# Kernel optimization log

Hardware: AMD Instinct MI355X
Metric: run time of the kernel (lower is better)

The kernel has to match this reference:

```python
import jax, jax.numpy as jnp
import numpy as np

HEADS = 8
DIM_HEAD = 64
SCALE = DIM_HEAD ** -0.5


def setup_inputs() -> dict:
    key = jax.random.key(0)
    k1, k2, k3, k4 = jax.random.split(key, 4)
    b, dim, l = 4, 512, 2048
    hidden = HEADS * DIM_HEAD  # 512
    x = jax.random.normal(k1, (b, dim, l), dtype=jnp.float32)
    w_qkv = jax.random.normal(k2, (3 * hidden, dim), dtype=jnp.float32) * (dim ** -0.5)
    w_out = jax.random.normal(k3, (dim, hidden), dtype=jnp.float32) * (hidden ** -0.5)
    b_out = jax.random.normal(k4, (dim,), dtype=jnp.float32) * 0.01
    return {"x": x, "w_qkv": w_qkv, "w_out": w_out, "b_out": b_out}


def reference(x, w_qkv, w_out, b_out):
    b, c, l = x.shape
    h, d = HEADS, DIM_HEAD
    # 1x1 Conv1d == channel matmul: [3*hidden, c] x [b, c, l] -> [b, 3*hidden, l]
    qkv = jnp.einsum('oc,bcl->bol', w_qkv, x)
    q, k, v = jnp.split(qkv, 3, axis=1)
    # 'b (h d) l -> b h d l'
    q = q.reshape(b, h, d, l) * SCALE
    k = k.reshape(b, h, d, l)
    v = v.reshape(b, h, d, l)
    sim = jnp.einsum('bhdi,bhdj->bhij', q, k)          # [b, h, l, l]
    attn = jax.nn.softmax(sim, axis=-1)
    out = jnp.einsum('bhij,bhdj->bhid', attn, v)       # [b, h, l, d]
    # 'b h l d -> b (h d) l'
    out = out.transpose(0, 1, 3, 2).reshape(b, h * d, l)
    return jnp.einsum('oc,bcl->bol', w_out, out) + b_out[None, :, None]
```

## Files before the change

kernel.cpp:

```cpp
#include <hip/hip_runtime.h>

#define L_SEQ 2048
#define KDIM  512

typedef __attribute__((ext_vector_type(8))) short short8v;
typedef __attribute__((ext_vector_type(4))) float f32x4;

static __device__ __forceinline__ short f2b(float f) {
    union { float f; unsigned u; } v; v.f = f;
    unsigned r = v.u + 0x7fffu + ((v.u >> 16) & 1u);
    return (short)(r >> 16);
}

static __device__ __forceinline__ float fast_exp2(float x) {
#if __has_builtin(__builtin_amdgcn_exp2f)
    return __builtin_amdgcn_exp2f(x);
#else
    return exp2f(x);
#endif
}

static __device__ __forceinline__ void gl2lds16(const short* g, short* l) {
    __builtin_amdgcn_global_load_lds(
        (const __attribute__((address_space(1))) unsigned*)g,
        (__attribute__((address_space(3))) unsigned*)l,
        16, 0, 0);
}

__global__ __launch_bounds__(256) void prep(
    const float* __restrict__ wq, const float* __restrict__ wo,
    const float* __restrict__ x,
    short* __restrict__ wqb, short* __restrict__ wob, short* __restrict__ xT)
{
    __shared__ __align__(16) float T[64 * 72];
    const int t = threadIdx.x;
    int bid = blockIdx.x;

    if (bid < 1024) {
        const int i = bid * 256 + t;
        const int NQ = 1536 * 512 / 4;
        float4 v;
        if (i < NQ) v = ((const float4*)wq)[i];
        else        v = ((const float4*)wo)[i - NQ];
        short4 s;
        s.x = f2b(v.x); s.y = f2b(v.y); s.z = f2b(v.z); s.w = f2b(v.w);
        if (i < NQ) ((short4*)wqb)[i] = s;
        else        ((short4*)wob)[i - NQ] = s;
        return;
    }
    bid -= 1024;
    const int l0 = (bid & 31) * 64;
    const int c0 = ((bid >> 5) & 7) * 64;
    const int b  = bid >> 8;

#pragma unroll
    for (int j = 0; j < 4; ++j) {
        const int idx = j * 256 + t;
        const int row = idx >> 4, c4 = idx & 15;
        const float4 v = *(const float4*)&x[((size_t)b * KDIM + c0 + row) * L_SEQ + l0 + c4 * 4];
        *(float4*)&T[row * 72 + c4 * 4] = v;
    }
    __syncthreads();

#pragma unroll
    for (int j = 0; j < 2; ++j) {
        const int idx = j * 256 + t;
        const int l = idx >> 3, ch = idx & 7;
        short8v s;
#pragma unroll
        for (int e = 0; e < 8; ++e)
            s[e] = f2b(T[(ch * 8 + e) * 72 + l]);
        *(short8v*)&xT[((size_t)b * L_SEQ + l0 + l) * KDIM + c0 + ch * 8] = s;
    }
}

template<int EPI>
__global__ __launch_bounds__(256) void gemm_bt(
    const short* __restrict__ Ag, const short* __restrict__ Bbase,
    const float* __restrict__ bias,
    short* __restrict__ Qws, short* __restrict__ Kws, short* __restrict__ Vws,
    float* __restrict__ Cout)
{
    constexpr int TO   = (EPI == 0) ? 128 : 64;
    constexpr int WO   = TO / 2;
    constexpr int NI   = WO / 16;
    constexpr int CA   = TO * 64 * 2 / 1024;
    constexpr int CB   = 16;
    constexpr int CPW  = (CA + CB) / 4;
    constexpr int SMEM = (EPI == 0) ? 34816 : 24576;

    const int bz = blockIdx.z;
    const int o0 = blockIdx.y * TO;
    const int l0 = blockIdx.x * 128;
    const short* Bg = Bbase + (size_t)bz * L_SEQ * KDIM;

    __shared__ __align__(16) char smem[SMEM];
    short* sA = (short*)smem;
    short* sB = (short*)(smem + TO * 64 * 2);

    const int t    = threadIdx.x;
    const int w    = t >> 6;
    const int lane = t & 63;
    const int quad = lane >> 4;
    const int l16  = lane & 15;
    const int wo   = (w & 1) * WO;
    const int wl   = (w >> 1) * 64;

    f32x4 acc[NI][4];
#pragma unroll
    for (int i = 0; i < NI; ++i)
#pragma unroll
        for (int n = 0; n < 4; ++n) acc[i][n] = (f32x4){0,0,0,0};

    const int lrow = lane >> 3;
    const int lcol = (lane & 7) * 8;

    for (int k0 = 0; k0 < KDIM; k0 += 64) {
#pragma unroll
        for (int p = 0; p < CPW; ++p) {
            const int cid = w * CPW + p;
            if (cid < CA) {
                const int row = cid * 8 + lrow;
                gl2lds16(Ag + (size_t)(o0 + row) * KDIM + k0 + lcol, sA + cid * 512);
            } else {
                const int row = (cid - CA) * 8 + lrow;
                gl2lds16(Bg + (size_t)(l0 + row) * KDIM + k0 + lcol, sB + (cid - CA) * 512);
            }
        }
        __syncthreads();

#pragma unroll
        for (int ks = 0; ks < 2; ++ks) {
            short8v af[NI], bf[4];
#pragma unroll
            for (int i = 0; i < NI; ++i)
                af[i] = *(const short8v*)&sA[(wo + i * 16 + l16) * 64 + ks * 32 + quad * 8];
#pragma unroll
            for (int n = 0; n < 4; ++n)
                bf[n] = *(const short8v*)&sB[(wl + n * 16 + l16) * 64 + ks * 32 + quad * 8];
#pragma unroll
            for (int i = 0; i < NI; ++i)
#pragma unroll
                for (int n = 0; n < 4; ++n)
                    acc[i][n] = __builtin_amdgcn_mfma_f32_16x16x32_bf16(af[i], bf[n], acc[i][n], 0, 0, 0);
        }
        __syncthreads();
    }

    if (EPI == 0) {
        const int type  = o0 >> 9;
        const int local = o0 & 511;
        const int bh0   = bz * 8 + (local >> 6);
        const float sc  = (type == 0) ? 0.18033688011112042f : 1.0f;
        short* T = (short*)smem;

        if (type == 2) {
#pragma unroll
            for (int i = 0; i < NI; ++i)
#pragma unroll
                for (int n = 0; n < 4; ++n)
#pragma unroll
                    for (int r = 0; r < 4; ++r)
                        T[(wo + i * 16 + quad * 4 + r) * 136 + wl + n * 16 + l16] =
                            f2b(acc[i][n][r]);
            __syncthreads();
#pragma unroll
            for (int p = 0; p < 8; ++p) {
                const int idx = p * 256 + t;
                const int o = idx >> 4, c = idx & 15;
                const float4 v = *(const float4*)&T[o * 136 + c * 8];
                short* dst = Vws + ((size_t)(bh0 + (o >> 6)) * 64 + (o & 63)) * L_SEQ + l0 + c * 8;
                *(float4*)dst = v;
            }
        } else {
#pragma unroll
            for (int i = 0; i < NI; ++i)
#pragma unroll
                for (int n = 0; n < 4; ++n) {
                    short4 s;
                    s.x = f2b(acc[i][n][0] * sc);
                    s.y = f2b(acc[i][n][1] * sc);
                    s.z = f2b(acc[i][n][2] * sc);
                    s.w = f2b(acc[i][n][3] * sc);
                    *(short4*)&T[(wl + n * 16 + l16) * 136 + wo + i * 16 + quad * 4] = s;
                }
            __syncthreads();
            short* base = (type == 0) ? Qws : Kws;
#pragma unroll
            for (int p = 0; p < 8; ++p) {
                const int idx = p * 256 + t;
                const int l = idx >> 4, c = idx & 15;
                const float4 v = *(const float4*)&T[l * 136 + c * 8];
                short* dst = base + ((size_t)(bh0 + (c >> 3)) * L_SEQ + l0 + l) * 64 + (c & 7) * 8;
                *(float4*)dst = v;
            }
        }
    } else {
        float* Cb = Cout + (size_t)bz * KDIM * L_SEQ;
#pragma unroll
        for (int i = 0; i < NI; ++i) {
            const int o = o0 + wo + i * 16 + quad * 4;
            float bv[4];
#pragma unroll
            for (int r = 0; r < 4; ++r) bv[r] = bias[o + r];
#pragma unroll
            for (int n = 0; n < 4; ++n) {
                const int l = l0 + wl + n * 16 + l16;
#pragma unroll
                for (int r = 0; r < 4; ++r)
                    Cb[(size_t)(o + r) * L_SEQ + l] = acc[i][n][r] + bv[r];
            }
        }
    }
}

__global__ __launch_bounds__(512) void attn_mfma(
    const short* __restrict__ Qws, const short* __restrict__ Kws,
    const short* __restrict__ Vws, short* __restrict__ ao)
{
    const int bh = blockIdx.x & 31;
    const int b  = bh >> 3;
    const int h  = bh & 7;
    const int i0 = (blockIdx.x >> 5) * 128;

    __shared__ __align__(16) char smem[55296];
    short* Pld = (short*)(smem + 36864);
    float* Old = (float*)smem;

    const int t    = threadIdx.x;
    const int w    = t >> 6;
    const int lane = t & 63;
    const int quad = lane >> 4;
    const int l16  = lane & 15;

    const short* Qb = Qws + (size_t)bh * L_SEQ * 64;
    const short* Kb = Kws + (size_t)bh * L_SEQ * 64;
    const short* Vb = Vws + (size_t)bh * 64 * L_SEQ;

    short8v qa0, qa1;
    {
        const short* qrow = Qb + (size_t)(i0 + w * 16 + l16) * 64 + quad * 8;
        qa0 = *(const short8v*)qrow;
        qa1 = *(const short8v*)(qrow + 32);
    }

    f32x4 oacc[4];
#pragma unroll
    for (int n = 0; n < 4; ++n) oacc[n] = (f32x4){0,0,0,0};
    float rsum = 0.f;
    short* Pw = Pld + w * 16 * 72;

    const int r = t >> 3, c = t & 7;

    {
        short* K0 = (short*)smem;
        short* V0 = (short*)(smem + 9216);
        const float4 k0 = *(const float4*)(Kb + (size_t)r * 64 + c * 8);
        const float4 v0 = *(const float4*)(Vb + (size_t)r * L_SEQ + c * 8);
        *(float4*)&K0[r * 72 + c * 8] = k0;
        *(float4*)&V0[r * 72 + c * 8] = v0;
    }
    __syncthreads();

    for (int jt = 0; jt < L_SEQ / 64; ++jt) {
        const int j0 = jt * 64;
        short* Kc = (short*)(smem + (jt & 1) * 18432);
        short* Vc = (short*)(smem + (jt & 1) * 18432 + 9216);
        const bool more = (jt + 1 < L_SEQ / 64);

        float4 nk, nv;
        if (more) {
            nk = *(const float4*)(Kb + (size_t)(j0 + 64 + r) * 64 + c * 8);
            nv = *(const float4*)(Vb + (size_t)r * L_SEQ + j0 + 64 + c * 8);
        }

        f32x4 sacc[4];
#pragma unroll
        for (int n = 0; n < 4; ++n) sacc[n] = (f32x4){0,0,0,0};
#pragma unroll
        for (int n = 0; n < 4; ++n) {
            const short8v kf0 = *(const short8v*)&Kc[(n * 16 + l16) * 72 + quad * 8];
            const short8v kf1 = *(const short8v*)&Kc[(n * 16 + l16) * 72 + 32 + quad * 8];
            sacc[n] = __builtin_amdgcn_mfma_f32_16x16x32_bf16(kf0, qa0, sacc[n], 0, 0, 0);
            sacc[n] = __builtin_amdgcn_mfma_f32_16x16x32_bf16(kf1, qa1, sacc[n], 0, 0, 0);
        }

#pragma unroll
        for (int n = 0; n < 4; ++n) {
            const float p0 = fast_exp2(sacc[n][0]);
            const float p1 = fast_exp2(sacc[n][1]);
            const float p2 = fast_exp2(sacc[n][2]);
            const float p3 = fast_exp2(sacc[n][3]);
            rsum += (p0 + p1) + (p2 + p3);
            uint2 pv;
            pv.x = __builtin_amdgcn_perm(__float_as_uint(p1), __float_as_uint(p0), 0x07060302u);
            pv.y = __builtin_amdgcn_perm(__float_as_uint(p3), __float_as_uint(p2), 0x07060302u);
            *(uint2*)&Pw[l16 * 72 + n * 16 + quad * 4] = pv;
        }

        const short8v pa0 = *(const short8v*)&Pw[l16 * 72 + quad * 8];
        const short8v pa1 = *(const short8v*)&Pw[l16 * 72 + 32 + quad * 8];
#pragma unroll
        for (int n = 0; n < 4; ++n) {
            const short8v vf0 = *(const short8v*)&Vc[(n * 16 + l16) * 72 + quad * 8];
            const short8v vf1 = *(const short8v*)&Vc[(n * 16 + l16) * 72 + 32 + quad * 8];
            oacc[n] = __builtin_amdgcn_mfma_f32_16x16x32_bf16(pa0, vf0, oacc[n], 0, 0, 0);
            oacc[n] = __builtin_amdgcn_mfma_f32_16x16x32_bf16(pa1, vf1, oacc[n], 0, 0, 0);
        }

        if (more) {
            short* Kn = (short*)(smem + ((jt & 1) ^ 1) * 18432);
            short* Vn = (short*)(smem + ((jt & 1) ^ 1) * 18432 + 9216);
            *(float4*)&Kn[r * 72 + c * 8] = nk;
            *(float4*)&Vn[r * 72 + c * 8] = nv;
        }
        __syncthreads();
    }

    rsum += __shfl_xor(rsum, 16, 64);
    rsum += __shfl_xor(rsum, 32, 64);
    const float inv = 1.0014f / rsum;

#pragma unroll
    for (int rr = 0; rr < 4; ++rr) {
        const float iv = __shfl(inv, quad * 4 + rr, 64);
#pragma unroll
        for (int n = 0; n < 4; ++n)
            Old[(w * 16 + quad * 4 + rr) * 68 + n * 16 + l16] = oacc[n][rr] * iv;
    }
    __syncthreads();
#pragma unroll
    for (int p = 0; p < 4; ++p) {
        const int idx = p * 512 + t;
        const int i = idx >> 4, c4 = idx & 15;
        const float4 v = *(const float4*)&Old[i * 68 + c4 * 4];
        short4 s;
        s.x = f2b(v.x); s.y = f2b(v.y); s.z = f2b(v.z); s.w = f2b(v.w);
        *(short4*)&ao[((size_t)b * L_SEQ + i0 + i) * KDIM + h * 64 + c4 * 4] = s;
    }
}

extern "C" void kernel_launch(void* const* d_in, const int* in_sizes, int n_in,
                              void* d_out, int out_size, void* d_ws, size_t ws_size,
                              hipStream_t stream)
{
    const float* x     = (const float*)d_in[0];
    const float* w_qkv = (const float*)d_in[1];
    const float* w_out = (const float*)d_in[2];
    const float* b_out = (const float*)d_in[3];
    float* out = (float*)d_out;

    char* ws = (char*)d_ws;
    short* xT    = (short*)ws;                      ws += (size_t)4 * L_SEQ * KDIM * 2;
    short* wq_bf = (short*)ws;                      ws += (size_t)1536 * 512 * 2;
    short* wo_bf = (short*)ws;                      ws += (size_t)512 * 512 * 2;
    short* Qws   = (short*)ws;                      ws += (size_t)32 * L_SEQ * 64 * 2;
    short* Kws   = (short*)ws;                      ws += (size_t)32 * L_SEQ * 64 * 2;
    short* Vws   = (short*)ws;                      ws += (size_t)32 * L_SEQ * 64 * 2;
    short* ao    = (short*)ws;

    dim3 blk(256);
    prep       <<<dim3(2048), blk, 0, stream>>>(w_qkv, w_out, x, wq_bf, wo_bf, xT);
    gemm_bt<0> <<<dim3(16, 12, 4), blk, 0, stream>>>(wq_bf, xT, nullptr, Qws, Kws, Vws, nullptr);
    attn_mfma  <<<dim3(512), dim3(512), 0, stream>>>(Qws, Kws, Vws, ao);
    gemm_bt<1> <<<dim3(16, 8, 4), blk, 0, stream>>>(wo_bf, ao, b_out, nullptr, nullptr, nullptr, out);
}
```

Baseline: 168.8 us.

## Switch attention to 32x32x16 MFMA with register-shuffled P and split-key warps

```diff
diff --git a/kernel.cpp b/kernel.cpp
--- a/kernel.cpp
+++ b/kernel.cpp
@@ -5,6 +5,8 @@
 
 typedef __attribute__((ext_vector_type(8))) short short8v;
 typedef __attribute__((ext_vector_type(4))) float f32x4;
+typedef __attribute__((ext_vector_type(16))) float f32x16;
+typedef __attribute__((ext_vector_type(4))) unsigned u32x4;
 
 static __device__ __forceinline__ short f2b(float f) {
     union { float f; unsigned u; } v; v.f = f;
@@ -214,7 +216,7 @@
     }
 }
 
-__global__ __launch_bounds__(512) void attn_mfma(
+__global__ __launch_bounds__(512, 4) void attn_mfma(
     const short* __restrict__ Qws, const short* __restrict__ Kws,
     const short* __restrict__ Vws, short* __restrict__ ao)
 {
@@ -223,32 +225,30 @@
     const int h  = bh & 7;
     const int i0 = (blockIdx.x >> 5) * 128;
 
-    __shared__ __align__(16) char smem[55296];
-    short* Pld = (short*)(smem + 36864);
+    __shared__ __align__(16) char smem[36864];
     float* Old = (float*)smem;
 
     const int t    = threadIdx.x;
     const int w    = t >> 6;
     const int lane = t & 63;
-    const int quad = lane >> 4;
-    const int l16  = lane & 15;
+    const int l31  = lane & 31;
+    const int hi   = lane >> 5;
+    const int gi   = w >> 1;
+    const int jh   = w & 1;
 
     const short* Qb = Qws + (size_t)bh * L_SEQ * 64;
     const short* Kb = Kws + (size_t)bh * L_SEQ * 64;
     const short* Vb = Vws + (size_t)bh * 64 * L_SEQ;
 
-    short8v qa0, qa1;
-    {
-        const short* qrow = Qb + (size_t)(i0 + w * 16 + l16) * 64 + quad * 8;
-        qa0 = *(const short8v*)qrow;
-        qa1 = *(const short8v*)(qrow + 32);
-    }
-
-    f32x4 oacc[4];
-#pragma unroll
-    for (int n = 0; n < 4; ++n) oacc[n] = (f32x4){0,0,0,0};
+    short8v qa[4];
+#pragma unroll
+    for (int dk = 0; dk < 4; ++dk)
+        qa[dk] = *(const short8v*)(Qb + (size_t)(i0 + gi * 32 + l31) * 64 + dk * 16 + hi * 8);
+
+    f32x16 oacc0, oacc1;
+#pragma unroll
+    for (int e = 0; e < 16; ++e) { oacc0[e] = 0.f; oacc1[e] = 0.f; }
     float rsum = 0.f;
-    short* Pw = Pld + w * 16 * 72;
 
     const int r = t >> 3, c = t & 7;
 
@@ -264,8 +264,8 @@
 
     for (int jt = 0; jt < L_SEQ / 64; ++jt) {
         const int j0 = jt * 64;
-        short* Kc = (short*)(smem + (jt & 1) * 18432);
-        short* Vc = (short*)(smem + (jt & 1) * 18432 + 9216);
+        const short* Kc = (const short*)(smem + (jt & 1) * 18432);
+        const short* Vc = (const short*)(smem + (jt & 1) * 18432 + 9216);
         const bool more = (jt + 1 < L_SEQ / 64);
 
         float4 nk, nv;
@@ -274,38 +274,52 @@
             nv = *(const float4*)(Vb + (size_t)r * L_SEQ + j0 + 64 + c * 8);
         }
 
-        f32x4 sacc[4];
-#pragma unroll
-        for (int n = 0; n < 4; ++n) sacc[n] = (f32x4){0,0,0,0};
-#pragma unroll
-        for (int n = 0; n < 4; ++n) {
-            const short8v kf0 = *(const short8v*)&Kc[(n * 16 + l16) * 72 + quad * 8];
-            const short8v kf1 = *(const short8v*)&Kc[(n * 16 + l16) * 72 + 32 + quad * 8];
-            sacc[n] = __builtin_amdgcn_mfma_f32_16x16x32_bf16(kf0, qa0, sacc[n], 0, 0, 0);
-            sacc[n] = __builtin_amdgcn_mfma_f32_16x16x32_bf16(kf1, qa1, sacc[n], 0, 0, 0);
-        }
-
-#pragma unroll
-        for (int n = 0; n < 4; ++n) {
-            const float p0 = fast_exp2(sacc[n][0]);
-            const float p1 = fast_exp2(sacc[n][1]);
-            const float p2 = fast_exp2(sacc[n][2]);
-            const float p3 = fast_exp2(sacc[n][3]);
-            rsum += (p0 + p1) + (p2 + p3);
-            uint2 pv;
-            pv.x = __builtin_amdgcn_perm(__float_as_uint(p1), __float_as_uint(p0), 0x07060302u);
-            pv.y = __builtin_amdgcn_perm(__float_as_uint(p3), __float_as_uint(p2), 0x07060302u);
-            *(uint2*)&Pw[l16 * 72 + n * 16 + quad * 4] = pv;
-        }
-
-        const short8v pa0 = *(const short8v*)&Pw[l16 * 72 + quad * 8];
-        const short8v pa1 = *(const short8v*)&Pw[l16 * 72 + 32 + quad * 8];
-#pragma unroll
-        for (int n = 0; n < 4; ++n) {
-            const short8v vf0 = *(const short8v*)&Vc[(n * 16 + l16) * 72 + quad * 8];
-            const short8v vf1 = *(const short8v*)&Vc[(n * 16 + l16) * 72 + 32 + quad * 8];
-            oacc[n] = __builtin_amdgcn_mfma_f32_16x16x32_bf16(pa0, vf0, oacc[n], 0, 0, 0);
-            oacc[n] = __builtin_amdgcn_mfma_f32_16x16x32_bf16(pa1, vf1, oacc[n], 0, 0, 0);
+        f32x16 sacc;
+#pragma unroll
+        for (int e = 0; e < 16; ++e) sacc[e] = 0.f;
+#pragma unroll
+        for (int dk = 0; dk < 4; ++dk) {
+            const short8v kf = *(const short8v*)&Kc[(jh * 32 + l31) * 72 + dk * 16 + hi * 8];
+            sacc = __builtin_amdgcn_mfma_f32_32x32x16_bf16(kf, qa[dk], sacc, 0, 0, 0);
+        }
+
+        float p[16];
+#pragma unroll
+        for (int e = 0; e < 16; ++e) p[e] = fast_exp2(sacc[e]);
+#pragma unroll
+        for (int e = 0; e < 16; e += 4)
+            rsum += (p[e] + p[e + 1]) + (p[e + 2] + p[e + 3]);
+
+        unsigned wv[8];
+#pragma unroll
+        for (int g = 0; g < 4; ++g) {
+            wv[2 * g]     = __builtin_amdgcn_perm(__float_as_uint(p[4 * g + 1]),
+                                                  __float_as_uint(p[4 * g]),     0x07060302u);
+            wv[2 * g + 1] = __builtin_amdgcn_perm(__float_as_uint(p[4 * g + 3]),
+                                                  __float_as_uint(p[4 * g + 2]), 0x07060302u);
+        }
+        unsigned xv[8];
+#pragma unroll
+        for (int k = 0; k < 8; ++k)
+            xv[k] = (unsigned)__shfl_xor((int)wv[k], 32, 64);
+
+        u32x4 f0, f1;
+        f0[0] = hi ? xv[2] : wv[0];  f0[1] = hi ? xv[3] : wv[1];
+        f0[2] = hi ? wv[2] : xv[0];  f0[3] = hi ? wv[3] : xv[1];
+        f1[0] = hi ? xv[6] : wv[4];  f1[1] = hi ? xv[7] : wv[5];
+        f1[2] = hi ? wv[6] : xv[4];  f1[3] = hi ? wv[7] : xv[5];
+        const short8v pa0 = __builtin_bit_cast(short8v, f0);
+        const short8v pa1 = __builtin_bit_cast(short8v, f1);
+
+        {
+            const short8v vf00 = *(const short8v*)&Vc[(0 * 32 + l31) * 72 + jh * 32 + 0 * 16 + hi * 8];
+            const short8v vf01 = *(const short8v*)&Vc[(1 * 32 + l31) * 72 + jh * 32 + 0 * 16 + hi * 8];
+            oacc0 = __builtin_amdgcn_mfma_f32_32x32x16_bf16(pa0, vf00, oacc0, 0, 0, 0);
+            oacc1 = __builtin_amdgcn_mfma_f32_32x32x16_bf16(pa0, vf01, oacc1, 0, 0, 0);
+            const short8v vf10 = *(const short8v*)&Vc[(0 * 32 + l31) * 72 + jh * 32 + 1 * 16 + hi * 8];
+            const short8v vf11 = *(const short8v*)&Vc[(1 * 32 + l31) * 72 + jh * 32 + 1 * 16 + hi * 8];
+            oacc0 = __builtin_amdgcn_mfma_f32_32x32x16_bf16(pa1, vf10, oacc0, 0, 0, 0);
+            oacc1 = __builtin_amdgcn_mfma_f32_32x32x16_bf16(pa1, vf11, oacc1, 0, 0, 0);
         }
 
         if (more) {
@@ -317,18 +331,55 @@
         __syncthreads();
     }
 
-    rsum += __shfl_xor(rsum, 16, 64);
-    rsum += __shfl_xor(rsum, 32, 64);
-    const float inv = 1.0014f / rsum;
-
-#pragma unroll
-    for (int rr = 0; rr < 4; ++rr) {
-        const float iv = __shfl(inv, quad * 4 + rr, 64);
-#pragma unroll
-        for (int n = 0; n < 4; ++n)
-            Old[(w * 16 + quad * 4 + rr) * 68 + n * 16 + l16] = oacc[n][rr] * iv;
+    const float r2 = rsum + __shfl_xor(rsum, 32, 64);
+
+    float* Opart = (float*)smem;
+    float* Rp    = (float*)(smem + 32768);
+
+    if (jh == 1) {
+#pragma unroll
+        for (int q = 0; q < 4; ++q) {
+            float4 a = { oacc0[4 * q], oacc0[4 * q + 1], oacc0[4 * q + 2], oacc0[4 * q + 3] };
+            float4 bq = { oacc1[4 * q], oacc1[4 * q + 1], oacc1[4 * q + 2], oacc1[4 * q + 3] };
+            *(float4*)&Opart[gi * 2048 + q * 256 + lane * 4]         = a;
+            *(float4*)&Opart[gi * 2048 + (4 + q) * 256 + lane * 4]   = bq;
+        }
+        if (hi == 0) Rp[gi * 32 + l31] = r2;
     }
     __syncthreads();
+
+    if (jh == 0) {
+#pragma unroll
+        for (int q = 0; q < 4; ++q) {
+            const float4 a  = *(const float4*)&Opart[gi * 2048 + q * 256 + lane * 4];
+            const float4 bq = *(const float4*)&Opart[gi * 2048 + (4 + q) * 256 + lane * 4];
+            oacc0[4 * q] += a.x;  oacc0[4 * q + 1] += a.y;
+            oacc0[4 * q + 2] += a.z; oacc0[4 * q + 3] += a.w;
+            oacc1[4 * q] += bq.x; oacc1[4 * q + 1] += bq.y;
+            oacc1[4 * q + 2] += bq.z; oacc1[4 * q + 3] += bq.w;
+        }
+        const float rt  = r2 + Rp[gi * 32 + l31];
+        const float inv = 1.0014f / rt;
+#pragma unroll
+        for (int e = 0; e < 16; ++e) {
+            const int rowi = (e & 3) + 8 * (e >> 2) + 4 * hi;
+            const float iv = __shfl(inv, rowi, 64);
+            oacc0[e] *= iv;
+            oacc1[e] *= iv;
+        }
+    }
+    __syncthreads();
+
+    if (jh == 0) {
+#pragma unroll
+        for (int e = 0; e < 16; ++e) {
+            const int rowi = (e & 3) + 8 * (e >> 2) + 4 * hi;
+            Old[(gi * 32 + rowi) * 68 + l31]      = oacc0[e];
+            Old[(gi * 32 + rowi) * 68 + 32 + l31] = oacc1[e];
+        }
+    }
+    __syncthreads();
+
 #pragma unroll
     for (int p = 0; p < 4; ++p) {
         const int idx = p * 512 + t;
```

Measured after the change: 162.1 us. 4.0% less time.
